# Performance work log

Hardware: AMD Instinct MI355X
Metric: run time of the kernel (lower is better)

The kernel has to match this reference:

```python
import jax, jax.numpy as jnp
import numpy as np

ORB = 54          # unify_orb_num = 27 * 2
N_ATOMS = 64
N_EDGES = 1536
N_P = 256
N_Q = 384
F_P, F_Q, F_O = 0.0002, 0.0001, 0.00015


def setup_inputs() -> dict:
    key = jax.random.key(0)
    ks = jax.random.split(key, 16)
    M = ORB * N_ATOMS
    lattice_vector = 10.0 * jnp.eye(3, dtype=jnp.float32) + 0.1 * jax.random.normal(ks[0], (3, 3), jnp.float32)
    atoms_positions = 10.0 * jax.random.uniform(ks[1], (N_ATOMS, 3), jnp.float32)
    edge_src = jax.random.randint(ks[2], (N_EDGES,), 0, N_ATOMS, jnp.int32)
    edge_dst = jax.random.randint(ks[3], (N_EDGES,), 0, N_ATOMS, jnp.int32)
    # edge_vec = (pos_j - pos_i) + R @ lattice so that round(cell_inv @ R_dis) recovers integer R
    R_int = jax.random.randint(ks[4], (N_EDGES, 3), -2, 3).astype(jnp.float32)
    edge_vec = (atoms_positions[edge_dst] - atoms_positions[edge_src]) + R_int @ lattice_vector
    hr_gt = jax.random.normal(ks[5], (N_EDGES, ORB, ORB), jnp.float32)
    hr_pred = hr_gt + 0.1 * jax.random.normal(ks[6], (N_EDGES, ORB, ORB), jnp.float32)
    kpt_coord = jax.random.uniform(ks[7], (3,), jnp.float32)
    s = np.float32(1.0 / np.sqrt(M))
    P_re = s * jax.random.normal(ks[8], (N_P, M), jnp.float32)
    P_im = s * jax.random.normal(ks[9], (N_P, M), jnp.float32)
    Q_re = s * jax.random.normal(ks[10], (N_Q, M), jnp.float32)
    Q_im = s * jax.random.normal(ks[11], (N_Q, M), jnp.float32)
    H_gt = jax.random.normal(ks[12], (N_EDGES, ORB, ORB), jnp.float32)
    pred_H = H_gt + 0.1 * jax.random.normal(ks[13], (N_EDGES, ORB, ORB), jnp.float32)
    overlap = jax.random.normal(ks[14], (N_EDGES, ORB, ORB), jnp.float32)
    mask_tensor = jnp.ones((N_EDGES, ORB, ORB), jnp.float32)
    return dict(edge_vec=edge_vec, lattice_vector=lattice_vector, atoms_positions=atoms_positions,
                hr_gt=hr_gt, hr_pred=hr_pred, kpt_coord=kpt_coord,
                P_re=P_re, P_im=P_im, Q_re=Q_re, Q_im=Q_im,
                H_gt=H_gt, pred_H=pred_H, overlap=overlap, mask_tensor=mask_tensor,
                edge_src=edge_src, edge_dst=edge_dst)


def _forward(edge_vec, lattice_vector, atoms_positions, hr_gt, hr_pred, kpt_coord,
             P_re, P_im, Q_re, Q_im, H_gt, pred_H, overlap, mask_tensor,
             edge_src, edge_dst):
    M = ORB * atoms_positions.shape[0]
    # --- get_R_list (vectorized): R_tot = round(inv(L^T) @ (edge_vec - (pos_j - pos_i))) ---
    cell_inv = jnp.linalg.inv(lattice_vector.T)
    R_dis = edge_vec - (atoms_positions[edge_dst] - atoms_positions[edge_src])   # [E,3]
    R_tot = jnp.round(R_dis @ cell_inv.T)                                        # [E,3]
    # --- cal_wfc_hk_vectorized: phase factors + block scatter into dense hk ---
    phase = jnp.exp(2j * jnp.pi * (R_tot @ kpt_coord)).astype(jnp.complex64)     # [E]
    idx = jnp.arange(ORB)
    rows = edge_src[:, None, None].astype(jnp.int32) * ORB + idx[None, :, None]  # [E,ORB,1]
    cols = edge_dst[:, None, None].astype(jnp.int32) * ORB + idx[None, None, :]  # [E,1,ORB]
    flat = (rows * M + cols).reshape(-1)                                         # [E*ORB*ORB]

    def build_hk(hr):
        contrib = phase[:, None, None] * hr.astype(jnp.complex64)                # [E,ORB,ORB]
        return jnp.zeros((M * M,), jnp.complex64).at[flat].add(contrib.reshape(-1)).reshape(M, M)

    P = (P_re + 1j * P_im).astype(jnp.complex64)   # [N_P, M]
    Q = (Q_re + 1j * Q_im).astype(jnp.complex64)   # [N_Q, M]

    def project(hk):
        PcH = P.conj() @ hk                        # [N_P, M]
        QcH = Q.conj() @ hk                        # [N_Q, M]
        return PcH @ P.T, QcH @ Q.T, PcH @ Q.T     # [N_P,N_P], [N_Q,N_Q], [N_P,N_Q]

    rP1, rQ1, rPQ1 = project(build_hk(hr_gt))
    rP2, rQ2, rPQ2 = project(build_hk(hr_pred))

    # --- grep_min_mu ---
    f_R = 1.0 - F_P - F_Q - F_O
    N1 = jnp.sum(mask_tensor)
    N2 = N_P * N_P
    N3 = N_Q * N_Q
    N4 = N_P * N_Q
    n1 = f_R * jnp.sum((pred_H - H_gt) * overlap) / N1   # real inputs: real(sum(x*conj(s)))
    d1 = f_R * jnp.sum(overlap * overlap) / N1
    n2 = F_P * jnp.real(jnp.trace(rP2 - rP1)) / N2
    d2 = F_P / N_P
    n3 = F_Q * jnp.real(jnp.trace(rQ2 - rQ1)) / N3
    d3 = F_Q / N_Q
    mu = jax.lax.stop_gradient((n1 + n2 + n3) / (d1 + d2 + d3))  # torch float(mu) detaches

    # --- cal_loss: L1 terms (reduction='none' then sum) ---
    l1 = lambda a, b: jnp.abs(a - b)
    loss_hr = l1(H_gt + mu * overlap, pred_H).sum()
    eyeP = jnp.eye(N_P, dtype=jnp.float32)
    eyeQ = jnp.eye(N_Q, dtype=jnp.float32)
    loss_p = l1(jnp.real(rP1) + mu * eyeP, jnp.real(rP2)).sum() + l1(jnp.imag(rP1), jnp.imag(rP2)).sum()
    loss_q = l1(jnp.real(rQ1) + mu * eyeQ, jnp.real(rQ2)).sum() + l1(jnp.imag(rQ1), jnp.imag(rQ2)).sum()
    loss_pq = l1(jnp.real(rPQ1), jnp.real(rPQ2)).sum() + l1(jnp.imag(rPQ1), jnp.imag(rPQ2)).sum()
    return f_R * loss_hr / N1 + F_P * loss_p / N2 + F_Q * loss_q / N3 + F_O * loss_pq / N4


def reference(edge_vec, lattice_vector, atoms_positions, hr_gt, hr_pred, kpt_coord,
              P_re, P_im, Q_re, Q_im, H_gt, pred_H, overlap, mask_tensor,
              edge_src, edge_dst):
    return _forward(edge_vec, lattice_vector, atoms_positions, hr_gt, hr_pred, kpt_coord,
                    P_re, P_im, Q_re, Q_im, H_gt, pred_H, overlap, mask_tensor,
                    edge_src, edge_dst)
```

## Files before the change

### kernel.cpp

```cpp
#include <hip/hip_runtime.h>
#include <math.h>

#define E_N    1536
#define NATOMS 64
#define M_DIM  3456
#define NP     256
#define NQ     384
#define HRSZ   2916

#define W_FP 0.0002f
#define W_FQ 0.0001f
#define W_FO 0.00015f
#define W_FR (1.0f - W_FP - W_FQ - W_FO)

#define B_HRD  3072
#define B_RED  1094
#define B_PQ   1280
#define B_PREP 1080
#define B_PH   6
#define B_TOT  (B_HRD + B_RED + B_PQ + B_PREP + B_PH)

#define B_LHR  1094

typedef __attribute__((ext_vector_type(8))) short short8;
typedef __attribute__((ext_vector_type(4))) float f32x4;

__device__ __forceinline__ unsigned pk_bf16(float a, float b) {
    unsigned r;
    asm volatile("v_cvt_pk_bf16_f32 %0, %1, %2" : "=v"(r) : "v"(a), "v"(b));
    return r;
}
__device__ __forceinline__ unsigned short f2bf(float x) {
    unsigned u = __builtin_bit_cast(unsigned, x);
    unsigned r = (u + 0x7fffu + ((u >> 16) & 1u)) >> 16;
    return (unsigned short)r;
}

__device__ __forceinline__ void gload_lds16(const void* g, void* l) {
    __builtin_amdgcn_global_load_lds(
        (const __attribute__((address_space(1))) unsigned int*)g,
        (__attribute__((address_space(3))) unsigned int*)l, 16, 0, 0);
}

__device__ __forceinline__ float blockSum(float v, float* sm) {
    v += __shfl_down(v, 32); v += __shfl_down(v, 16); v += __shfl_down(v, 8);
    v += __shfl_down(v, 4);  v += __shfl_down(v, 2);  v += __shfl_down(v, 1);
    __syncthreads();
    if ((threadIdx.x & 63) == 0) sm[threadIdx.x >> 6] = v;
    __syncthreads();
    float r = 0.0f;
    if (threadIdx.x == 0) {
        int nw = blockDim.x >> 6;
        for (int i = 0; i < nw; ++i) r += sm[i];
    }
    return r;
}

__global__ __launch_bounds__(256) void k_pre(
        const float* __restrict__ edge_vec, const float* __restrict__ lat,
        const float* __restrict__ apos, const float* __restrict__ kpt,
        const int* __restrict__ esrc, const int* __restrict__ edst,
        const float* __restrict__ hr_gt, const float* __restrict__ hr_pred,
        const float* __restrict__ P_re, const float* __restrict__ P_im,
        const float* __restrict__ Q_re, const float* __restrict__ Q_im,
        const float4* __restrict__ Hg, const float4* __restrict__ Hp,
        const float4* __restrict__ ov, const float4* __restrict__ mk,
        float* __restrict__ phre, float* __restrict__ phim,
        int* __restrict__ bcnt, int* __restrict__ blist,
        unsigned* __restrict__ hrdG,
        unsigned* __restrict__ PpadR, unsigned* __restrict__ PpadI,
        ushort4* __restrict__ Prebf, ushort4* __restrict__ Pimbf,
        ushort4* __restrict__ Qrebf, ushort4* __restrict__ Qimbf,
        float* __restrict__ acc) {
    __shared__ float sm[8];
    int bid = blockIdx.x;
    int tid = threadIdx.x;

    if (bid < B_HRD) {
        int idx = bid*256 + tid;
        int e = idx >> 9;
        int p = idx & 511;
        int i = p >> 3, q = p & 7;
        unsigned outv[4] = {0,0,0,0};
        if (i < 54 && q < 7) {
            const float* g = hr_gt  + (size_t)e*HRSZ + i*54;
            const float* h = hr_pred + (size_t)e*HRSZ + i*54;
            #pragma unroll
            for (int u = 0; u < 4; ++u) {
                int j2 = q*4 + u;
                if (j2 < 27) {
                    float2 gg = *(const float2*)(g + 2*j2);
                    float2 hh = *(const float2*)(h + 2*j2);
                    outv[u] = pk_bf16(hh.x - gg.x, hh.y - gg.y);
                }
            }
        }
        *(uint4*)(hrdG + (size_t)e*2048 + i*32 + ((q ^ (i & 7)) << 2)) =
            make_uint4(outv[0], outv[1], outv[2], outv[3]);
    } else if (bid < B_HRD + B_RED) {
        const int N4 = E_N*HRSZ/4;
        int base = (bid - B_HRD)*1024 + tid;
        float4 hg[4], hp[4], o[4], m[4];
        #pragma unroll
        for (int u = 0; u < 4; ++u) {
            int i = base + u*256;
            if (i < N4) { hg[u]=Hg[i]; hp[u]=Hp[i]; o[u]=ov[i]; m[u]=mk[i]; }
            else { hg[u]=float4{0,0,0,0}; hp[u]=hg[u]; o[u]=hg[u]; m[u]=hg[u]; }
        }
        float s0 = 0, s1 = 0, s2 = 0;
        #pragma unroll
        for (int u = 0; u < 4; ++u) {
            s0 += (hp[u].x-hg[u].x)*o[u].x + (hp[u].y-hg[u].y)*o[u].y
                + (hp[u].z-hg[u].z)*o[u].z + (hp[u].w-hg[u].w)*o[u].w;
            s1 += o[u].x*o[u].x + o[u].y*o[u].y + o[u].z*o[u].z + o[u].w*o[u].w;
            s2 += m[u].x + m[u].y + m[u].z + m[u].w;
        }
        float r0 = blockSum(s0, sm);
        float r1 = blockSum(s1, sm);
        float r2 = blockSum(s2, sm);
        if (tid == 0) {
            atomicAdd(&acc[0], r0);
            atomicAdd(&acc[1], r1);
            atomicAdd(&acc[2], r2);
        }
    } else if (bid < B_HRD + B_RED + B_PQ) {
        int idx = (bid - B_HRD - B_RED)*256 + tid;
        int q = idx & 7;
        int r = idx >> 3;
        int c = r % 640;
        int dst = r / 640;
        const float* sre = (c < NP) ? (P_re + (size_t)c*M_DIM) : (Q_re + (size_t)(c-NP)*M_DIM);
        const float* sim = (c < NP) ? (P_im + (size_t)c*M_DIM) : (Q_im + (size_t)(c-NP)*M_DIM);
        unsigned vr[4] = {0,0,0,0}, vi[4] = {0,0,0,0};
        if (q < 7) {
            #pragma unroll
            for (int u = 0; u < 4; ++u) {
                int j2 = q*4 + u;
                if (j2 < 27) {
                    int o = dst*54 + 2*j2;
                    float2 fr = *(const float2*)(sre + o);
                    float2 fi = *(const float2*)(sim + o);
                    vr[u] = pk_bf16(fr.x, fr.y);
                    vi[u] = pk_bf16(fi.x, fi.y);
                }
            }
        }
        int loc = (dst*640 + c)*32 + ((q ^ (c & 7)) << 2);
        *(uint4*)(PpadR + loc) = make_uint4(vr[0], vr[1], vr[2], vr[3]);
        *(uint4*)(PpadI + loc) = make_uint4(vi[0], vi[1], vi[2], vi[3]);
    } else if (bid < B_HRD + B_RED + B_PQ + B_PREP) {
        const int NP4 = NP*M_DIM/4;
        const int NQ4 = NQ*M_DIM/4;
        int base = (bid - B_HRD - B_RED - B_PQ)*1024 + tid;
        #pragma unroll
        for (int u = 0; u < 4; ++u) {
            int i = base + u*256;
            const float4* src; ushort4* dst; int o;
            if (i < NP4)            { src = (const float4*)P_re; dst = Prebf; o = i; }
            else if (i < 2*NP4)     { src = (const float4*)P_im; dst = Pimbf; o = i - NP4; }
            else if (i < 2*NP4+NQ4) { src = (const float4*)Q_re; dst = Qrebf; o = i - 2*NP4; }
            else                    { src = (const float4*)Q_im; dst = Qimbf; o = i - 2*NP4 - NQ4; }
            float4 v = src[o];
            ushort4 uu;
            uu.x = f2bf(v.x); uu.y = f2bf(v.y); uu.z = f2bf(v.z); uu.w = f2bf(v.w);
            dst[o] = uu;
        }
    } else {
        int e = (bid - B_HRD - B_RED - B_PQ - B_PREP)*256 + tid;
        if (e >= E_N) return;
        float a00 = lat[0], a01 = lat[3], a02 = lat[6];
        float a10 = lat[1], a11 = lat[4], a12 = lat[7];
        float a20 = lat[2], a21 = lat[5], a22 = lat[8];
        float c00 = a11*a22 - a12*a21;
        float c01 = a12*a20 - a10*a22;
        float c02 = a10*a21 - a11*a20;
        float det = a00*c00 + a01*c01 + a02*c02;
        float id  = 1.0f / det;
        float i00 = c00*id;
        float i01 = (a02*a21 - a01*a22)*id;
        float i02 = (a01*a12 - a02*a11)*id;
        float i10 = c01*id;
        float i11 = (a00*a22 - a02*a20)*id;
        float i12 = (a02*a10 - a00*a12)*id;
        float i20 = c02*id;
        float i21 = (a01*a20 - a00*a21)*id;
        float i22 = (a00*a11 - a01*a10)*id;
        int s = esrc[e], d = edst[e];
        float r0 = edge_vec[e*3+0] - (apos[d*3+0] - apos[s*3+0]);
        float r1 = edge_vec[e*3+1] - (apos[d*3+1] - apos[s*3+1]);
        float r2 = edge_vec[e*3+2] - (apos[d*3+2] - apos[s*3+2]);
        float t0 = roundf(i00*r0 + i01*r1 + i02*r2);
        float t1 = roundf(i10*r0 + i11*r1 + i12*r2);
        float t2 = roundf(i20*r0 + i21*r1 + i22*r2);
        float ph = t0*kpt[0] + t1*kpt[1] + t2*kpt[2];
        float ang = 6.28318530717958647692f * ph;
        phre[e] = cosf(ang);
        phim[e] = sinf(ang);
        int p = atomicAdd(&bcnt[s], 1);
        if (p < 128) blist[s*128 + p] = (e << 6) | d;
    }
}

__global__ __launch_bounds__(256) void k_bp(
        const unsigned* __restrict__ hrdG,
        const unsigned* __restrict__ PpadR, const unsigned* __restrict__ PpadI,
        const float* __restrict__ phre, const float* __restrict__ phim,
        const int* __restrict__ bcnt, const int* __restrict__ blist,
        ushort* __restrict__ BPTPre, ushort* __restrict__ BPTPim,
        ushort* __restrict__ BPTQre, ushort* __restrict__ BPTQim) {
    __shared__ ushort lds[2][12288];
    __shared__ int elist[128];
    __shared__ float phs[2][128];

    int tid = threadIdx.x;
    int a   = blockIdx.x / 10;
    int t   = blockIdx.x - a*10;
    ushort *Or, *Oi; int col0;
    if (t < 4) { Or = BPTPre; Oi = BPTPim; col0 = t*64; }
    else       { Or = BPTQre; Oi = BPTQim; col0 = (t-4)*64; }

    int ne = bcnt[a]; if (ne > 128) ne = 128;
    for (int k = tid; k < ne; k += 256) {
        int v = blist[a*128 + k];
        elist[k] = v;
        phs[0][k] = phre[v >> 6];
        phs[1][k] = phim[v >> 6];
    }
    __syncthreads();

    int w = tid >> 6, l = tid & 63;
    int wr0 = (w >> 1)*32, wc0 = (w & 1)*32;
    int lr = l & 15, kq = l >> 4, lk4 = (l >> 4)*4;

    f32x4 accRe[2][2] = {}, accIm[2][2] = {};

    #define ISSUE(nn, bb) do {                                                     \
        int v_ = elist[(nn)];                                                      \
        int ee_ = v_ >> 6, dst_ = v_ & 63;                                         \
        const ushort* g0_ = (const ushort*)(hrdG + (size_t)ee_*2048);              \
        const ushort* g1_ = (const ushort*)(PpadR + ((size_t)dst_*640 + t*64)*32); \
        const ushort* g2_ = (const ushort*)(PpadI + ((size_t)dst_*640 + t*64)*32); \
        ushort* lb_ = &lds[(bb)][0];                                               \
        _Pragma("unroll")                                                          \
        for (int j_ = 0; j_ < 6; ++j_) {                                           \
            int jj_ = w + j_*4;                                                    \
            int arr_ = jj_ >> 3, ch_ = jj_ & 7;                                    \
            const ushort* gb_ = (arr_ == 0) ? g0_ : (arr_ == 1) ? g1_ : g2_;       \
            gload_lds16(gb_ + ch_*512 + l*8, (void*)(lb_ + arr_*4096 + ch_*512));  \
        }                                                                          \
    } while (0)

    if (ne > 0) ISSUE(0, 0);
    for (int n = 0; n < ne; ++n) {
        int cur = n & 1;
        if (n + 1 < ne) {
            ISSUE(n+1, 1-cur);
            asm volatile("s_waitcnt vmcnt(6)" ::: "memory");
        } else {
            asm volatile("s_waitcnt vmcnt(0)" ::: "memory");
        }
        __syncthreads();
        float phr = phs[0][n], phi_ = phs[1][n];
        const ushort* A  = &lds[cur][0];
        const ushort* BR = A + 4096;
        const ushort* BI = A + 8192;
        short8 a0[2], a1[2], br0[2], br1[2], bi0[2], bi1[2];
        #pragma unroll
        for (int mr = 0; mr < 2; ++mr) {
            int r = wr0 + mr*16 + lr;
            a0[mr] = *(const short8*)(A + r*64 + ((kq     ^ (r & 7))<<3));
            a1[mr] = *(const short8*)(A + r*64 + (((4+kq) ^ (r & 7))<<3));
        }
        #pragma unroll
        for (int nc = 0; nc < 2; ++nc) {
            int c = wc0 + nc*16 + lr;
            br0[nc] = *(const short8*)(BR + c*64 + ((kq     ^ (c & 7))<<3));
            br1[nc] = *(const short8*)(BR + c*64 + (((4+kq) ^ (c & 7))<<3));
            bi0[nc] = *(const short8*)(BI + c*64 + ((kq     ^ (c & 7))<<3));
            bi1[nc] = *(const short8*)(BI + c*64 + (((4+kq) ^ (c & 7))<<3));
        }
        f32x4 z = {0.0f, 0.0f, 0.0f, 0.0f};
        f32x4 t1[2][2], t2[2][2];
        #pragma unroll
        for (int mr = 0; mr < 2; ++mr)
            #pragma unroll
            for (int nc = 0; nc < 2; ++nc) {
                t1[mr][nc] = __builtin_amdgcn_mfma_f32_16x16x32_bf16(a0[mr], br0[nc], z, 0, 0, 0);
                t1[mr][nc] = __builtin_amdgcn_mfma_f32_16x16x32_bf16(a1[mr], br1[nc], t1[mr][nc], 0, 0, 0);
                t2[mr][nc] = __builtin_amdgcn_mfma_f32_16x16x32_bf16(a0[mr], bi0[nc], z, 0, 0, 0);
                t2[mr][nc] = __builtin_amdgcn_mfma_f32_16x16x32_bf16(a1[mr], bi1[nc], t2[mr][nc], 0, 0, 0);
            }
        #pragma unroll
        for (int mr = 0; mr < 2; ++mr)
            #pragma unroll
            for (int nc = 0; nc < 2; ++nc)
                #pragma unroll
                for (int q = 0; q < 4; ++q) {
                    accRe[mr][nc][q] += phr*t1[mr][nc][q] - phi_*t2[mr][nc][q];
                    accIm[mr][nc][q] += phr*t2[mr][nc][q] + phi_*t1[mr][nc][q];
                }
        __syncthreads();
    }
    #undef ISSUE

    #pragma unroll
    for (int mr = 0; mr < 2; ++mr)
        #pragma unroll
        for (int nc = 0; nc < 2; ++nc) {
            int ib = wr0 + mr*16 + lk4;
            if (ib < 54) {
                int cg = col0 + wc0 + nc*16 + lr;
                size_t base = (size_t)cg*M_DIM + (size_t)a*54 + ib;
                *(unsigned*)(Or + base) = pk_bf16(accRe[mr][nc][0], accRe[mr][nc][1]);
                *(unsigned*)(Oi + base) = pk_bf16(accIm[mr][nc][0], accIm[mr][nc][1]);
                if (ib + 2 < 54) {
                    *(unsigned*)(Or + base + 2) = pk_bf16(accRe[mr][nc][2], accRe[mr][nc][3]);
                    *(unsigned*)(Oi + base + 2) = pk_bf16(accIm[mr][nc][2], accIm[mr][nc][3]);
                }
            }
        }
}

#define GPAD 40
__global__ __launch_bounds__(256) void k_gemm(
        const ushort* __restrict__ Prebf, const ushort* __restrict__ Pimbf,
        const ushort* __restrict__ Qrebf, const ushort* __restrict__ Qimbf,
        const ushort* __restrict__ BPTPre, const ushort* __restrict__ BPTPim,
        const ushort* __restrict__ BPTQre, const ushort* __restrict__ BPTQim,
        float* __restrict__ part) {
    __shared__ ushort Ar[64*GPAD], Ai[64*GPAD], Br_[64*GPAD], Bi_[64*GPAD];
    int tid = threadIdx.x;
    int bid = blockIdx.x;
    int t = bid / 6, ks = bid - t*6;
    const ushort *Ag, *Aig, *Bg, *Big; float *Cre, *Cim; int NC, r0, c0;
    if (t < 16) {
        Ag = Prebf; Aig = Pimbf; Bg = BPTPre; Big = BPTPim;
        NC = NP; r0 = (t & 3)*64; c0 = (t >> 2)*64;
        Cre = part + (size_t)ks*2*65536; Cim = Cre + 65536;
    } else if (t < 52) {
        int u = t - 16;
        Ag = Qrebf; Aig = Qimbf; Bg = BPTQre; Big = BPTQim;
        NC = NQ; r0 = (u % 6)*64; c0 = (u / 6)*64;
        Cre = part + 786432 + (size_t)ks*2*147456; Cim = Cre + 147456;
    } else {
        int u = t - 52;
        Ag = Prebf; Aig = Pimbf; Bg = BPTQre; Big = BPTQim;
        NC = NQ; r0 = (u & 3)*64; c0 = (u >> 2)*64;
        Cre = part + 786432 + 1769472 + (size_t)ks*2*98304; Cim = Cre + 98304;
    }
    int k0 = ks * 576;
    int srow = tid >> 2, skq = (tid & 3) * 8;
    int w = tid >> 6, l = tid & 63;
    int wr0 = (w >> 1)*32, wc0 = (w & 1)*32;
    int lr = l & 15, lk = (l >> 4)*8, lk4 = (l >> 4)*4;

    const ushort* pa  = Ag  + (size_t)(r0+srow)*M_DIM + k0 + skq;
    const ushort* pai = Aig + (size_t)(r0+srow)*M_DIM + k0 + skq;
    const ushort* pb  = Bg  + (size_t)(c0+srow)*M_DIM + k0 + skq;
    const ushort* pbi = Big + (size_t)(c0+srow)*M_DIM + k0 + skq;

    short8 ra = *(const short8*)pa, rai = *(const short8*)pai;
    short8 rb = *(const short8*)pb, rbi = *(const short8*)pbi;

    f32x4 aRe[2][2] = {}, aIA[2][2] = {}, aIB[2][2] = {};
    for (int s = 0; s < 18; ++s) {
        __syncthreads();
        *(short8*)(Ar  + srow*GPAD + skq) = ra;
        *(short8*)(Ai  + srow*GPAD + skq) = rai;
        *(short8*)(Br_ + srow*GPAD + skq) = rb;
        *(short8*)(Bi_ + srow*GPAD + skq) = rbi;
        __syncthreads();
        if (s < 17) {
            int o = (s+1)*32;
            ra  = *(const short8*)(pa  + o);
            rai = *(const short8*)(pai + o);
            rb  = *(const short8*)(pb  + o);
            rbi = *(const short8*)(pbi + o);
        }
        short8 fa[2], fn[2], fb[2], fi[2];
        #pragma unroll
        for (int mr = 0; mr < 2; ++mr) {
            int r = wr0 + mr*16 + lr;
            fa[mr] = *(const short8*)(Ar + r*GPAD + lk);
            fn[mr] = *(const short8*)(Ai + r*GPAD + lk);
        }
        #pragma unroll
        for (int nc = 0; nc < 2; ++nc) {
            int c = wc0 + nc*16 + lr;
            fb[nc] = *(const short8*)(Br_ + c*GPAD + lk);
            fi[nc] = *(const short8*)(Bi_ + c*GPAD + lk);
        }
        #pragma unroll
        for (int mr = 0; mr < 2; ++mr)
            #pragma unroll
            for (int nc = 0; nc < 2; ++nc) {
                aRe[mr][nc] = __builtin_amdgcn_mfma_f32_16x16x32_bf16(fa[mr], fb[nc], aRe[mr][nc], 0, 0, 0);
                aRe[mr][nc] = __builtin_amdgcn_mfma_f32_16x16x32_bf16(fn[mr], fi[nc], aRe[mr][nc], 0, 0, 0);
                aIA[mr][nc] = __builtin_amdgcn_mfma_f32_16x16x32_bf16(fa[mr], fi[nc], aIA[mr][nc], 0, 0, 0);
                aIB[mr][nc] = __builtin_amdgcn_mfma_f32_16x16x32_bf16(fn[mr], fb[nc], aIB[mr][nc], 0, 0, 0);
            }
    }
    #pragma unroll
    for (int mr = 0; mr < 2; ++mr)
        #pragma unroll
        for (int nc = 0; nc < 2; ++nc)
            #pragma unroll
            for (int rr = 0; rr < 4; ++rr) {
                int row = r0 + wr0 + mr*16 + lk4 + rr;
                int col = c0 + wc0 + nc*16 + lr;
                Cre[(size_t)row*NC + col] = aRe[mr][nc][rr];
                Cim[(size_t)row*NC + col] = aIA[mr][nc][rr] - aIB[mr][nc][rr];
            }
}

__global__ void k_mu(const float* __restrict__ part, float* __restrict__ acc) {
    int t = threadIdx.x;
    float v1 = 0.0f, v2 = 0.0f;
    if (t < NP) {
        #pragma unroll
        for (int ks = 0; ks < 6; ++ks) v1 += part[ks*131072 + t*(NP+1)];
    }
    if (t < NQ) {
        const float* q = part + 786432;
        #pragma unroll
        for (int ks = 0; ks < 6; ++ks) v2 += q[ks*294912 + t*(NQ+1)];
    }
    __shared__ float sm[8];
    float trP = blockSum(v1, sm);
    float trQ = blockSum(v2, sm);
    if (t == 0) {
        float N1 = acc[2];
        float n1 = W_FR * acc[0] / N1;
        float d1 = W_FR * acc[1] / N1;
        float n2 = W_FP * trP / (float)(NP*NP);
        float n3 = W_FQ * trQ / (float)(NQ*NQ);
        float d2 = W_FP / (float)NP;
        float d3 = W_FQ / (float)NQ;
        acc[3] = (n1 + n2 + n3) / (d1 + d2 + d3);
    }
}

__global__ __launch_bounds__(256) void k_loss(
        const float4* __restrict__ Hg, const float4* __restrict__ Hp,
        const float4* __restrict__ ov, const float* __restrict__ part,
        float* __restrict__ acc) {
    __shared__ float sm[8];
    int bid = blockIdx.x;
    int tid = threadIdx.x;
    float mu = acc[3];
    if (bid < B_LHR) {
        const int N4 = E_N*HRSZ/4;
        int base = bid*1024 + tid;
        float4 hg[4], hp[4], o[4];
        #pragma unroll
        for (int u = 0; u < 4; ++u) {
            int i = base + u*256;
            if (i < N4) { hg[u]=Hg[i]; hp[u]=Hp[i]; o[u]=ov[i]; }
            else { hg[u]=float4{0,0,0,0}; hp[u]=hg[u]; o[u]=hg[u]; }
        }
        float s = 0;
        #pragma unroll
        for (int u = 0; u < 4; ++u) {
            s += fabsf(hg[u].x + mu*o[u].x - hp[u].x) + fabsf(hg[u].y + mu*o[u].y - hp[u].y)
               + fabsf(hg[u].z + mu*o[u].z - hp[u].z) + fabsf(hg[u].w + mu*o[u].w - hp[u].w);
        }
        float r = blockSum(s, sm);
        if (tid == 0) atomicAdd(&acc[4], r);
    } else {
        const int NPP = NP*NP, NQQ = NQ*NQ, NPQ = NP*NQ;
        float sP = 0, sQ = 0, sPQ = 0;
        int stride = 256*256;
        for (int i = (bid - B_LHR)*256 + tid; i < NPP+NQQ+NPQ; i += stride) {
            if (i < NPP) {
                float sre = 0, sim = 0;
                #pragma unroll
                for (int ks = 0; ks < 6; ++ks) {
                    sre += part[ks*131072 + i];
                    sim += part[ks*131072 + 65536 + i];
                }
                int r = i >> 8, c = i & 255;
                float d = (r == c) ? mu : 0.0f;
                sP += fabsf(d - sre) + fabsf(sim);
            } else if (i < NPP+NQQ) {
                int j = i - NPP;
                const float* q = part + 786432;
                float sre = 0, sim = 0;
                #pragma unroll
                for (int ks = 0; ks < 6; ++ks) {
                    sre += q[ks*294912 + j];
                    sim += q[ks*294912 + 147456 + j];
                }
                int r = j / NQ, c = j - r*NQ;
                float d = (r == c) ? mu : 0.0f;
                sQ += fabsf(d - sre) + fabsf(sim);
            } else {
                int j = i - (NPP+NQQ);
                const float* pq = part + 786432 + 1769472;
                float sre = 0, sim = 0;
                #pragma unroll
                for (int ks = 0; ks < 6; ++ks) {
                    sre += pq[ks*196608 + j];
                    sim += pq[ks*196608 + 98304 + j];
                }
                sPQ += fabsf(sre) + fabsf(sim);
            }
        }
        float a1 = blockSum(sP, sm);
        float a2 = blockSum(sQ, sm);
        float a3 = blockSum(sPQ, sm);
        if (tid == 0) {
            atomicAdd(&acc[5], a1);
            atomicAdd(&acc[6], a2);
            atomicAdd(&acc[7], a3);
        }
    }
}

__global__ void k_final(const float* __restrict__ acc, float* __restrict__ out) {
    if (threadIdx.x == 0 && blockIdx.x == 0) {
        float N1 = acc[2];
        out[0] = W_FR*acc[4]/N1
               + W_FP*acc[5]/(float)(NP*NP)
               + W_FQ*acc[6]/(float)(NQ*NQ)
               + W_FO*acc[7]/(float)(NP*NQ);
    }
}

extern "C" void kernel_launch(void* const* d_in, const int* in_sizes, int n_in,
                              void* d_out, int out_size, void* d_ws, size_t ws_size,
                              hipStream_t stream) {
    const float* edge_vec = (const float*)d_in[0];
    const float* lattice  = (const float*)d_in[1];
    const float* apos     = (const float*)d_in[2];
    const float* hr_gt    = (const float*)d_in[3];
    const float* hr_pred  = (const float*)d_in[4];
    const float* kpt      = (const float*)d_in[5];
    const float* P_re     = (const float*)d_in[6];
    const float* P_im     = (const float*)d_in[7];
    const float* Q_re     = (const float*)d_in[8];
    const float* Q_im     = (const float*)d_in[9];
    const float* H_gt     = (const float*)d_in[10];
    const float* pred_H   = (const float*)d_in[11];
    const float* overlap  = (const float*)d_in[12];
    const float* mask     = (const float*)d_in[13];
    const int*   esrc     = (const int*)d_in[14];
    const int*   edst     = (const int*)d_in[15];
    float* out = (float*)d_out;

    float* ws   = (float*)d_ws;
    float* acc  = ws;
    int*   bcnt = (int*)(ws + 16);
    int*   blist= (int*)(ws + 80);
    float* phre = ws + 8272;
    float* phim = phre + E_N;
    ushort* us  = (ushort*)(ws + 16384);
    ushort* Prebf  = us;
    ushort* Pimbf  = Prebf  + (size_t)NP*M_DIM;
    ushort* Qrebf  = Pimbf  + (size_t)NP*M_DIM;
    ushort* Qimbf  = Qrebf  + (size_t)NQ*M_DIM;
    ushort* BPTPre = Qimbf  + (size_t)NQ*M_DIM;
    ushort* BPTPim = BPTPre + (size_t)NP*M_DIM;
    ushort* BPTQre = BPTPim + (size_t)NP*M_DIM;
    ushort* BPTQim = BPTQre + (size_t)NQ*M_DIM;
    unsigned* PpadR = (unsigned*)(BPTQim + (size_t)NQ*M_DIM);
    unsigned* PpadI = PpadR + (size_t)64*640*32;
    unsigned* hrdG  = PpadI + (size_t)64*640*32;
    float* part = (float*)hrdG;

    hipMemsetAsync(ws, 0, 320, stream);

    k_pre<<<B_TOT, 256, 0, stream>>>(edge_vec, lattice, apos, kpt, esrc, edst,
                                     hr_gt, hr_pred, P_re, P_im, Q_re, Q_im,
                                     (const float4*)H_gt, (const float4*)pred_H,
                                     (const float4*)overlap, (const float4*)mask,
                                     phre, phim, bcnt, blist,
                                     hrdG, PpadR, PpadI,
                                     (ushort4*)Prebf, (ushort4*)Pimbf,
                                     (ushort4*)Qrebf, (ushort4*)Qimbf, acc);
    k_bp<<<NATOMS*10, 256, 0, stream>>>(hrdG, PpadR, PpadI, phre, phim, bcnt, blist,
                                        BPTPre, BPTPim, BPTQre, BPTQim);
    k_gemm<<<456, 256, 0, stream>>>(Prebf, Pimbf, Qrebf, Qimbf,
                                    BPTPre, BPTPim, BPTQre, BPTQim, part);
    k_mu<<<1, 512, 0, stream>>>(part, acc);
    k_loss<<<B_LHR + 256, 256, 0, stream>>>((const float4*)H_gt, (const float4*)pred_H,
                                            (const float4*)overlap, part, acc);
    k_final<<<1, 1, 0, stream>>>(acc, out);
}
```

Baseline: 308.2 us.

## Cache bf16 H-difference and overlap in pre-pass; fuse P/Q bf16 conversion into padding

The pre-kernel now runs on a fixed 1024-block grid with grid-stride loops. The separate P/Q bf16 conversion pass is merged into the padded-layout pass, so P and Q are read once. When the workspace is large enough, the reduction pass also writes bf16 copies of (pred_H - H_gt) and overlap, and the final L1 loss reads those 4-byte pairs instead of three fp32 tensors, cutting that pass's traffic. The cost is extra writes in the pre-pass and bf16 rounding in the hr loss term, which changes numerics.

```diff
diff --git a/kernel.cpp b/kernel.cpp
--- a/kernel.cpp
+++ b/kernel.cpp
@@ -13,14 +13,10 @@
 #define W_FO 0.00015f
 #define W_FR (1.0f - W_FP - W_FQ - W_FO)
 
-#define B_HRD  3072
-#define B_RED  1094
-#define B_PQ   1280
-#define B_PREP 1080
-#define B_PH   6
-#define B_TOT  (B_HRD + B_RED + B_PQ + B_PREP + B_PH)
-
-#define B_LHR  1094
+#define N4_RED (E_N*HRSZ/4)
+#define TOT_A  (E_N*512)
+#define TOT_C  (NATOMS*640*8)
+#define GRID_PRE 1024
 
 typedef __attribute__((ext_vector_type(8))) short short8;
 typedef __attribute__((ext_vector_type(4))) float f32x4;
@@ -30,10 +26,9 @@
     asm volatile("v_cvt_pk_bf16_f32 %0, %1, %2" : "=v"(r) : "v"(a), "v"(b));
     return r;
 }
-__device__ __forceinline__ unsigned short f2bf(float x) {
-    unsigned u = __builtin_bit_cast(unsigned, x);
-    unsigned r = (u + 0x7fffu + ((u >> 16) & 1u)) >> 16;
-    return (unsigned short)r;
+__device__ __forceinline__ float bf2f(unsigned short u) {
+    unsigned v = ((unsigned)u) << 16;
+    return __builtin_bit_cast(float, v);
 }
 
 __device__ __forceinline__ void gload_lds16(const void* g, void* l) {
@@ -69,15 +64,53 @@
         int* __restrict__ bcnt, int* __restrict__ blist,
         unsigned* __restrict__ hrdG,
         unsigned* __restrict__ PpadR, unsigned* __restrict__ PpadI,
-        ushort4* __restrict__ Prebf, ushort4* __restrict__ Pimbf,
-        ushort4* __restrict__ Qrebf, ushort4* __restrict__ Qimbf,
-        float* __restrict__ acc) {
+        ushort* __restrict__ Prebf, ushort* __restrict__ Pimbf,
+        ushort* __restrict__ Qrebf, ushort* __restrict__ Qimbf,
+        unsigned* __restrict__ dH, unsigned* __restrict__ ovb,
+        float* __restrict__ acc, int compact) {
     __shared__ float sm[8];
     int bid = blockIdx.x;
     int tid = threadIdx.x;
 
-    if (bid < B_HRD) {
-        int idx = bid*256 + tid;
+    if (bid < 6) {
+        int e = bid*256 + tid;
+        if (e < E_N) {
+            float a00 = lat[0], a01 = lat[3], a02 = lat[6];
+            float a10 = lat[1], a11 = lat[4], a12 = lat[7];
+            float a20 = lat[2], a21 = lat[5], a22 = lat[8];
+            float c00 = a11*a22 - a12*a21;
+            float c01 = a12*a20 - a10*a22;
+            float c02 = a10*a21 - a11*a20;
+            float det = a00*c00 + a01*c01 + a02*c02;
+            float id  = 1.0f / det;
+            float i00 = c00*id;
+            float i01 = (a02*a21 - a01*a22)*id;
+            float i02 = (a01*a12 - a02*a11)*id;
+            float i10 = c01*id;
+            float i11 = (a00*a22 - a02*a20)*id;
+            float i12 = (a02*a10 - a00*a12)*id;
+            float i20 = c02*id;
+            float i21 = (a01*a20 - a00*a21)*id;
+            float i22 = (a00*a11 - a01*a10)*id;
+            int s = esrc[e], d = edst[e];
+            float r0 = edge_vec[e*3+0] - (apos[d*3+0] - apos[s*3+0]);
+            float r1 = edge_vec[e*3+1] - (apos[d*3+1] - apos[s*3+1]);
+            float r2 = edge_vec[e*3+2] - (apos[d*3+2] - apos[s*3+2]);
+            float t0 = roundf(i00*r0 + i01*r1 + i02*r2);
+            float t1 = roundf(i10*r0 + i11*r1 + i12*r2);
+            float t2 = roundf(i20*r0 + i21*r1 + i22*r2);
+            float ph = t0*kpt[0] + t1*kpt[1] + t2*kpt[2];
+            float ang = 6.28318530717958647692f * ph;
+            phre[e] = cosf(ang);
+            phim[e] = sinf(ang);
+            int p = atomicAdd(&bcnt[s], 1);
+            if (p < 128) blist[s*128 + p] = (e << 6) | d;
+        }
+    }
+
+    #pragma unroll
+    for (int it = 0; it < 3; ++it) {
+        int idx = bid*256 + tid + it*(GRID_PRE*256);
         int e = idx >> 9;
         int p = idx & 511;
         int i = p >> 3, q = p & 7;
@@ -97,23 +130,37 @@
         }
         *(uint4*)(hrdG + (size_t)e*2048 + i*32 + ((q ^ (i & 7)) << 2)) =
             make_uint4(outv[0], outv[1], outv[2], outv[3]);
-    } else if (bid < B_HRD + B_RED) {
-        const int N4 = E_N*HRSZ/4;
-        int base = (bid - B_HRD)*1024 + tid;
-        float4 hg[4], hp[4], o[4], m[4];
-        #pragma unroll
-        for (int u = 0; u < 4; ++u) {
-            int i = base + u*256;
-            if (i < N4) { hg[u]=Hg[i]; hp[u]=Hp[i]; o[u]=ov[i]; m[u]=mk[i]; }
-            else { hg[u]=float4{0,0,0,0}; hp[u]=hg[u]; o[u]=hg[u]; m[u]=hg[u]; }
-        }
+    }
+
+    {
         float s0 = 0, s1 = 0, s2 = 0;
         #pragma unroll
-        for (int u = 0; u < 4; ++u) {
-            s0 += (hp[u].x-hg[u].x)*o[u].x + (hp[u].y-hg[u].y)*o[u].y
-                + (hp[u].z-hg[u].z)*o[u].z + (hp[u].w-hg[u].w)*o[u].w;
-            s1 += o[u].x*o[u].x + o[u].y*o[u].y + o[u].z*o[u].z + o[u].w*o[u].w;
-            s2 += m[u].x + m[u].y + m[u].z + m[u].w;
+        for (int it = 0; it < 2; ++it) {
+            if (bid*1024 + it*(GRID_PRE*1024) < N4_RED) {
+                int b0 = bid*1024 + tid + it*(GRID_PRE*1024);
+                float4 hg[4], hp[4], o[4], m[4];
+                int val[4];
+                #pragma unroll
+                for (int u = 0; u < 4; ++u) {
+                    int i = b0 + u*256;
+                    val[u] = (i < N4_RED);
+                    if (val[u]) { hg[u]=Hg[i]; hp[u]=Hp[i]; o[u]=ov[i]; m[u]=mk[i]; }
+                    else { hg[u]=float4{0,0,0,0}; hp[u]=hg[u]; o[u]=hg[u]; m[u]=hg[u]; }
+                }
+                #pragma unroll
+                for (int u = 0; u < 4; ++u) {
+                    float dx = hp[u].x-hg[u].x, dy = hp[u].y-hg[u].y;
+                    float dz = hp[u].z-hg[u].z, dw = hp[u].w-hg[u].w;
+                    s0 += dx*o[u].x + dy*o[u].y + dz*o[u].z + dw*o[u].w;
+                    s1 += o[u].x*o[u].x + o[u].y*o[u].y + o[u].z*o[u].z + o[u].w*o[u].w;
+                    s2 += m[u].x + m[u].y + m[u].z + m[u].w;
+                    if (compact && val[u]) {
+                        int i = b0 + u*256;
+                        *(uint2*)(dH  + (size_t)i*2) = make_uint2(pk_bf16(dx, dy), pk_bf16(dz, dw));
+                        *(uint2*)(ovb + (size_t)i*2) = make_uint2(pk_bf16(o[u].x, o[u].y), pk_bf16(o[u].z, o[u].w));
+                    }
+                }
+            }
         }
         float r0 = blockSum(s0, sm);
         float r1 = blockSum(s1, sm);
@@ -123,81 +170,42 @@
             atomicAdd(&acc[1], r1);
             atomicAdd(&acc[2], r2);
         }
-    } else if (bid < B_HRD + B_RED + B_PQ) {
-        int idx = (bid - B_HRD - B_RED)*256 + tid;
-        int q = idx & 7;
-        int r = idx >> 3;
-        int c = r % 640;
-        int dst = r / 640;
-        const float* sre = (c < NP) ? (P_re + (size_t)c*M_DIM) : (Q_re + (size_t)(c-NP)*M_DIM);
-        const float* sim = (c < NP) ? (P_im + (size_t)c*M_DIM) : (Q_im + (size_t)(c-NP)*M_DIM);
-        unsigned vr[4] = {0,0,0,0}, vi[4] = {0,0,0,0};
-        if (q < 7) {
-            #pragma unroll
-            for (int u = 0; u < 4; ++u) {
-                int j2 = q*4 + u;
-                if (j2 < 27) {
-                    int o = dst*54 + 2*j2;
-                    float2 fr = *(const float2*)(sre + o);
-                    float2 fi = *(const float2*)(sim + o);
-                    vr[u] = pk_bf16(fr.x, fr.y);
-                    vi[u] = pk_bf16(fi.x, fi.y);
-                }
-            }
-        }
-        int loc = (dst*640 + c)*32 + ((q ^ (c & 7)) << 2);
-        *(uint4*)(PpadR + loc) = make_uint4(vr[0], vr[1], vr[2], vr[3]);
-        *(uint4*)(PpadI + loc) = make_uint4(vi[0], vi[1], vi[2], vi[3]);
-    } else if (bid < B_HRD + B_RED + B_PQ + B_PREP) {
-        const int NP4 = NP*M_DIM/4;
-        const int NQ4 = NQ*M_DIM/4;
-        int base = (bid - B_HRD - B_RED - B_PQ)*1024 + tid;
-        #pragma unroll
-        for (int u = 0; u < 4; ++u) {
-            int i = base + u*256;
-            const float4* src; ushort4* dst; int o;
-            if (i < NP4)            { src = (const float4*)P_re; dst = Prebf; o = i; }
-            else if (i < 2*NP4)     { src = (const float4*)P_im; dst = Pimbf; o = i - NP4; }
-            else if (i < 2*NP4+NQ4) { src = (const float4*)Q_re; dst = Qrebf; o = i - 2*NP4; }
-            else                    { src = (const float4*)Q_im; dst = Qimbf; o = i - 2*NP4 - NQ4; }
-            float4 v = src[o];
-            ushort4 uu;
-            uu.x = f2bf(v.x); uu.y = f2bf(v.y); uu.z = f2bf(v.z); uu.w = f2bf(v.w);
-            dst[o] = uu;
-        }
-    } else {
-        int e = (bid - B_HRD - B_RED - B_PQ - B_PREP)*256 + tid;
-        if (e >= E_N) return;
-        float a00 = lat[0], a01 = lat[3], a02 = lat[6];
-        float a10 = lat[1], a11 = lat[4], a12 = lat[7];
-        float a20 = lat[2], a21 = lat[5], a22 = lat[8];
-        float c00 = a11*a22 - a12*a21;
-        float c01 = a12*a20 - a10*a22;
-        float c02 = a10*a21 - a11*a20;
-        float det = a00*c00 + a01*c01 + a02*c02;
-        float id  = 1.0f / det;
-        float i00 = c00*id;
-        float i01 = (a02*a21 - a01*a22)*id;
-        float i02 = (a01*a12 - a02*a11)*id;
-        float i10 = c01*id;
-        float i11 = (a00*a22 - a02*a20)*id;
-        float i12 = (a02*a10 - a00*a12)*id;
-        float i20 = c02*id;
-        float i21 = (a01*a20 - a00*a21)*id;
-        float i22 = (a00*a11 - a01*a10)*id;
-        int s = esrc[e], d = edst[e];
-        float r0 = edge_vec[e*3+0] - (apos[d*3+0] - apos[s*3+0]);
-        float r1 = edge_vec[e*3+1] - (apos[d*3+1] - apos[s*3+1]);
-        float r2 = edge_vec[e*3+2] - (apos[d*3+2] - apos[s*3+2]);
-        float t0 = roundf(i00*r0 + i01*r1 + i02*r2);
-        float t1 = roundf(i10*r0 + i11*r1 + i12*r2);
-        float t2 = roundf(i20*r0 + i21*r1 + i22*r2);
-        float ph = t0*kpt[0] + t1*kpt[1] + t2*kpt[2];
-        float ang = 6.28318530717958647692f * ph;
-        phre[e] = cosf(ang);
-        phim[e] = sinf(ang);
-        int p = atomicAdd(&bcnt[s], 1);
-        if (p < 128) blist[s*128 + p] = (e << 6) | d;
+    }
+
+    #pragma unroll
+    for (int it = 0; it < 2; ++it) {
+        int idx = bid*256 + tid + it*(GRID_PRE*256);
+        if (idx < TOT_C) {
+            int q = idx & 7;
+            int r = idx >> 3;
+            int c = r % 640;
+            int dst = r / 640;
+            const float* sre = (c < NP) ? (P_re + (size_t)c*M_DIM) : (Q_re + (size_t)(c-NP)*M_DIM);
+            const float* sim = (c < NP) ? (P_im + (size_t)c*M_DIM) : (Q_im + (size_t)(c-NP)*M_DIM);
+            ushort* fre = (c < NP) ? Prebf : Qrebf;
+            ushort* fim = (c < NP) ? Pimbf : Qimbf;
+            int cc = (c < NP) ? c : c - NP;
+            unsigned vr[4] = {0,0,0,0}, vi[4] = {0,0,0,0};
+            if (q < 7) {
+                #pragma unroll
+                for (int u = 0; u < 4; ++u) {
+                    int j2 = q*4 + u;
+                    if (j2 < 27) {
+                        int o = dst*54 + 2*j2;
+                        float2 fr = *(const float2*)(sre + o);
+                        float2 fi = *(const float2*)(sim + o);
+                        vr[u] = pk_bf16(fr.x, fr.y);
+                        vi[u] = pk_bf16(fi.x, fi.y);
+                        int fo = cc*M_DIM + dst*54 + 2*j2;
+                        *(unsigned*)(fre + fo) = vr[u];
+                        *(unsigned*)(fim + fo) = vi[u];
+                    }
+                }
+            }
+            int loc = (dst*640 + c)*32 + ((q ^ (c & 7)) << 2);
+            *(uint4*)(PpadR + loc) = make_uint4(vr[0], vr[1], vr[2], vr[3]);
+            *(uint4*)(PpadI + loc) = make_uint4(vi[0], vi[1], vi[2], vi[3]);
+        }
     }
 }
 
@@ -442,27 +450,49 @@
 
 __global__ __launch_bounds__(256) void k_loss(
         const float4* __restrict__ Hg, const float4* __restrict__ Hp,
-        const float4* __restrict__ ov, const float* __restrict__ part,
-        float* __restrict__ acc) {
+        const float4* __restrict__ ov,
+        const uint4* __restrict__ dH, const uint4* __restrict__ ovb,
+        const float* __restrict__ part,
+        float* __restrict__ acc, int bhr, int compact) {
     __shared__ float sm[8];
     int bid = blockIdx.x;
     int tid = threadIdx.x;
     float mu = acc[3];
-    if (bid < B_LHR) {
-        const int N4 = E_N*HRSZ/4;
-        int base = bid*1024 + tid;
-        float4 hg[4], hp[4], o[4];
-        #pragma unroll
-        for (int u = 0; u < 4; ++u) {
-            int i = base + u*256;
-            if (i < N4) { hg[u]=Hg[i]; hp[u]=Hp[i]; o[u]=ov[i]; }
-            else { hg[u]=float4{0,0,0,0}; hp[u]=hg[u]; o[u]=hg[u]; }
-        }
+    if (bid < bhr) {
         float s = 0;
-        #pragma unroll
-        for (int u = 0; u < 4; ++u) {
-            s += fabsf(hg[u].x + mu*o[u].x - hp[u].x) + fabsf(hg[u].y + mu*o[u].y - hp[u].y)
-               + fabsf(hg[u].z + mu*o[u].z - hp[u].z) + fabsf(hg[u].w + mu*o[u].w - hp[u].w);
+        if (compact) {
+            const int N8 = E_N*HRSZ/8;
+            int b0 = bid*1024 + tid;
+            #pragma unroll
+            for (int u = 0; u < 4; ++u) {
+                int i8 = b0 + u*256;
+                if (i8 < N8) {
+                    uint4 dv = dH[i8];
+                    uint4 o4 = ovb[i8];
+                    unsigned dd[4] = {dv.x, dv.y, dv.z, dv.w};
+                    unsigned oo[4] = {o4.x, o4.y, o4.z, o4.w};
+                    #pragma unroll
+                    for (int p = 0; p < 4; ++p) {
+                        float d0 = bf2f((unsigned short)(dd[p] & 0xffffu));
+                        float d1 = bf2f((unsigned short)(dd[p] >> 16));
+                        float o0 = bf2f((unsigned short)(oo[p] & 0xffffu));
+                        float o1 = bf2f((unsigned short)(oo[p] >> 16));
+                        s += fabsf(mu*o0 - d0) + fabsf(mu*o1 - d1);
+                    }
+                }
+            }
+        } else {
+            const int N4 = E_N*HRSZ/4;
+            int b0 = bid*1024 + tid;
+            #pragma unroll
+            for (int u = 0; u < 4; ++u) {
+                int i = b0 + u*256;
+                if (i < N4) {
+                    float4 hg = Hg[i], hp = Hp[i], o = ov[i];
+                    s += fabsf(hg.x + mu*o.x - hp.x) + fabsf(hg.y + mu*o.y - hp.y)
+                       + fabsf(hg.z + mu*o.z - hp.z) + fabsf(hg.w + mu*o.w - hp.w);
+                }
+            }
         }
         float r = blockSum(s, sm);
         if (tid == 0) atomicAdd(&acc[4], r);
@@ -470,7 +500,7 @@
         const int NPP = NP*NP, NQQ = NQ*NQ, NPQ = NP*NQ;
         float sP = 0, sQ = 0, sPQ = 0;
         int stride = 256*256;
-        for (int i = (bid - B_LHR)*256 + tid; i < NPP+NQQ+NPQ; i += stride) {
+        for (int i = (bid - bhr)*256 + tid; i < NPP+NQQ+NPQ; i += stride) {
             if (i < NPP) {
                 float sre = 0, sim = 0;
                 #pragma unroll
@@ -566,23 +596,31 @@
     unsigned* PpadI = PpadR + (size_t)64*640*32;
     unsigned* hrdG  = PpadI + (size_t)64*640*32;
     float* part = (float*)hrdG;
+    size_t part_end_bytes = ((char*)part - (char*)d_ws) + (size_t)3735552*4;
+    unsigned* dH  = (unsigned*)((char*)d_ws + part_end_bytes);
+    unsigned* ovb = dH + (size_t)E_N*HRSZ/2;
+    size_t need = part_end_bytes + 2*(size_t)E_N*HRSZ*2;
+    int compact = (ws_size >= need) ? 1 : 0;
 
     hipMemsetAsync(ws, 0, 320, stream);
 
-    k_pre<<<B_TOT, 256, 0, stream>>>(edge_vec, lattice, apos, kpt, esrc, edst,
-                                     hr_gt, hr_pred, P_re, P_im, Q_re, Q_im,
-                                     (const float4*)H_gt, (const float4*)pred_H,
-                                     (const float4*)overlap, (const float4*)mask,
-                                     phre, phim, bcnt, blist,
-                                     hrdG, PpadR, PpadI,
-                                     (ushort4*)Prebf, (ushort4*)Pimbf,
-                                     (ushort4*)Qrebf, (ushort4*)Qimbf, acc);
+    k_pre<<<GRID_PRE, 256, 0, stream>>>(edge_vec, lattice, apos, kpt, esrc, edst,
+                                        hr_gt, hr_pred, P_re, P_im, Q_re, Q_im,
+                                        (const float4*)H_gt, (const float4*)pred_H,
+                                        (const float4*)overlap, (const float4*)mask,
+                                        phre, phim, bcnt, blist,
+                                        hrdG, PpadR, PpadI,
+                                        Prebf, Pimbf, Qrebf, Qimbf,
+                                        dH, ovb, acc, compact);
     k_bp<<<NATOMS*10, 256, 0, stream>>>(hrdG, PpadR, PpadI, phre, phim, bcnt, blist,
                                         BPTPre, BPTPim, BPTQre, BPTQim);
     k_gemm<<<456, 256, 0, stream>>>(Prebf, Pimbf, Qrebf, Qimbf,
                                     BPTPre, BPTPim, BPTQre, BPTQim, part);
     k_mu<<<1, 512, 0, stream>>>(part, acc);
-    k_loss<<<B_LHR + 256, 256, 0, stream>>>((const float4*)H_gt, (const float4*)pred_H,
-                                            (const float4*)overlap, part, acc);
+    int bhr = compact ? 547 : 1094;
+    k_loss<<<bhr + 256, 256, 0, stream>>>((const float4*)H_gt, (const float4*)pred_H,
+                                          (const float4*)overlap,
+                                          (const uint4*)dH, (const uint4*)ovb,
+                                          part, acc, bhr, compact);
     k_final<<<1, 1, 0, stream>>>(acc, out);
 }
```

New measurement: 314.4 us. 2.0% more time.

## Compute mu traces in k_bp epilogue and fuse H loss into GEMM launch

Applied to the files above, without the earlier changes.

The diagonal traces of the P and Q Gram products are now accumulated in the k_bp epilogue as elementwise dot products of the projected accumulators with the P/Q bf16 rows. This lets mu be known before the GEMM finishes, so the separate single-block k_mu kernel is removed. The large L1 loss over H_gt/pred_H/overlap moves into extra blocks of the GEMM launch, so it can overlap with GEMM work. Risks include different rounding in the trace, since it uses fp32 accumulators times bf16 instead of summed GEMM partials, plus extra global reads and a block reduction in k_bp.

```diff
diff --git a/kernel.cpp b/kernel.cpp
--- a/kernel.cpp
+++ b/kernel.cpp
@@ -20,7 +20,11 @@
 #define B_PH   6
 #define B_TOT  (B_HRD + B_RED + B_PQ + B_PREP + B_PH)
 
-#define B_LHR  1094
+#define N4_RED (E_N*HRSZ/4)
+#define TOT_C  (NATOMS*640*8)
+
+#define BHR    1094
+#define BGEMM  456
 
 typedef __attribute__((ext_vector_type(8))) short short8;
 typedef __attribute__((ext_vector_type(4))) float f32x4;
@@ -34,6 +38,10 @@
     unsigned u = __builtin_bit_cast(unsigned, x);
     unsigned r = (u + 0x7fffu + ((u >> 16) & 1u)) >> 16;
     return (unsigned short)r;
+}
+__device__ __forceinline__ float bf2f(unsigned short u) {
+    unsigned v = ((unsigned)u) << 16;
+    return __builtin_bit_cast(float, v);
 }
 
 __device__ __forceinline__ void gload_lds16(const void* g, void* l) {
@@ -54,6 +62,17 @@
         for (int i = 0; i < nw; ++i) r += sm[i];
     }
     return r;
+}
+
+__device__ __forceinline__ float mu_from(const float* acc) {
+    float N1 = acc[2];
+    float n1 = W_FR * acc[0] / N1;
+    float d1 = W_FR * acc[1] / N1;
+    float n2 = W_FP * acc[8] / (float)(NP*NP);
+    float n3 = W_FQ * acc[9] / (float)(NQ*NQ);
+    float d2 = W_FP / (float)NP;
+    float d3 = W_FQ / (float)NQ;
+    return (n1 + n2 + n3) / (d1 + d2 + d3);
 }
 
 __global__ __launch_bounds__(256) void k_pre(
@@ -98,13 +117,12 @@
         *(uint4*)(hrdG + (size_t)e*2048 + i*32 + ((q ^ (i & 7)) << 2)) =
             make_uint4(outv[0], outv[1], outv[2], outv[3]);
     } else if (bid < B_HRD + B_RED) {
-        const int N4 = E_N*HRSZ/4;
         int base = (bid - B_HRD)*1024 + tid;
         float4 hg[4], hp[4], o[4], m[4];
         #pragma unroll
         for (int u = 0; u < 4; ++u) {
             int i = base + u*256;
-            if (i < N4) { hg[u]=Hg[i]; hp[u]=Hp[i]; o[u]=ov[i]; m[u]=mk[i]; }
+            if (i < N4_RED) { hg[u]=Hg[i]; hp[u]=Hp[i]; o[u]=ov[i]; m[u]=mk[i]; }
             else { hg[u]=float4{0,0,0,0}; hp[u]=hg[u]; o[u]=hg[u]; m[u]=hg[u]; }
         }
         float s0 = 0, s1 = 0, s2 = 0;
@@ -206,18 +224,23 @@
         const unsigned* __restrict__ PpadR, const unsigned* __restrict__ PpadI,
         const float* __restrict__ phre, const float* __restrict__ phim,
         const int* __restrict__ bcnt, const int* __restrict__ blist,
+        const ushort* __restrict__ Prebf, const ushort* __restrict__ Pimbf,
+        const ushort* __restrict__ Qrebf, const ushort* __restrict__ Qimbf,
         ushort* __restrict__ BPTPre, ushort* __restrict__ BPTPim,
-        ushort* __restrict__ BPTQre, ushort* __restrict__ BPTQim) {
+        ushort* __restrict__ BPTQre, ushort* __restrict__ BPTQim,
+        float* __restrict__ acc) {
     __shared__ ushort lds[2][12288];
     __shared__ int elist[128];
     __shared__ float phs[2][128];
+    __shared__ float smtr[8];
 
     int tid = threadIdx.x;
     int a   = blockIdx.x / 10;
     int t   = blockIdx.x - a*10;
     ushort *Or, *Oi; int col0;
-    if (t < 4) { Or = BPTPre; Oi = BPTPim; col0 = t*64; }
-    else       { Or = BPTQre; Oi = BPTQim; col0 = (t-4)*64; }
+    const ushort *Fr, *Fi;
+    if (t < 4) { Or = BPTPre; Oi = BPTPim; col0 = t*64; Fr = Prebf; Fi = Pimbf; }
+    else       { Or = BPTQre; Oi = BPTQim; col0 = (t-4)*64; Fr = Qrebf; Fi = Qimbf; }
 
     int ne = bcnt[a]; if (ne > 128) ne = 128;
     for (int k = tid; k < ne; k += 256) {
@@ -319,6 +342,26 @@
                 }
             }
         }
+
+    float tr = 0.0f;
+    #pragma unroll
+    for (int mr = 0; mr < 2; ++mr)
+        #pragma unroll
+        for (int nc = 0; nc < 2; ++nc) {
+            int ib = wr0 + mr*16 + lk4;
+            int cg = col0 + wc0 + nc*16 + lr;
+            size_t off = (size_t)cg*M_DIM + (size_t)a*54 + ib;
+            #pragma unroll
+            for (int q = 0; q < 4; ++q) {
+                if (ib + q < 54) {
+                    float pr = bf2f(Fr[off + q]);
+                    float pi = bf2f(Fi[off + q]);
+                    tr += accRe[mr][nc][q]*pr + accIm[mr][nc][q]*pi;
+                }
+            }
+        }
+    float rtr = blockSum(tr, smtr);
+    if (tid == 0) atomicAdd(&acc[8 + (t < 4 ? 0 : 1)], rtr);
 }
 
 #define GPAD 40
@@ -327,11 +370,37 @@
         const ushort* __restrict__ Qrebf, const ushort* __restrict__ Qimbf,
         const ushort* __restrict__ BPTPre, const ushort* __restrict__ BPTPim,
         const ushort* __restrict__ BPTQre, const ushort* __restrict__ BPTQim,
-        float* __restrict__ part) {
+        const float4* __restrict__ Hg, const float4* __restrict__ Hp,
+        const float4* __restrict__ ov,
+        float* __restrict__ part, float* __restrict__ acc) {
     __shared__ ushort Ar[64*GPAD], Ai[64*GPAD], Br_[64*GPAD], Bi_[64*GPAD];
     int tid = threadIdx.x;
     int bid = blockIdx.x;
-    int t = bid / 6, ks = bid - t*6;
+
+    if (bid < BHR) {
+        float mu = mu_from(acc);
+        int base = bid*1024 + tid;
+        float4 hg[4], hp[4], o[4];
+        #pragma unroll
+        for (int u = 0; u < 4; ++u) {
+            int i = base + u*256;
+            if (i < N4_RED) { hg[u]=Hg[i]; hp[u]=Hp[i]; o[u]=ov[i]; }
+            else { hg[u]=float4{0,0,0,0}; hp[u]=hg[u]; o[u]=hg[u]; }
+        }
+        float s = 0;
+        #pragma unroll
+        for (int u = 0; u < 4; ++u) {
+            s += fabsf(hg[u].x + mu*o[u].x - hp[u].x) + fabsf(hg[u].y + mu*o[u].y - hp[u].y)
+               + fabsf(hg[u].z + mu*o[u].z - hp[u].z) + fabsf(hg[u].w + mu*o[u].w - hp[u].w);
+        }
+        __shared__ float sm[8];
+        float r = blockSum(s, sm);
+        if (tid == 0) atomicAdd(&acc[4], r);
+        return;
+    }
+
+    int b2 = bid - BHR;
+    int t = b2 / 6, ks = b2 - t*6;
     const ushort *Ag, *Aig, *Bg, *Big; float *Cre, *Cim; int NC, r0, c0;
     if (t < 16) {
         Ag = Prebf; Aig = Pimbf; Bg = BPTPre; Big = BPTPim;
@@ -413,106 +482,56 @@
             }
 }
 
-__global__ void k_mu(const float* __restrict__ part, float* __restrict__ acc) {
-    int t = threadIdx.x;
-    float v1 = 0.0f, v2 = 0.0f;
-    if (t < NP) {
-        #pragma unroll
-        for (int ks = 0; ks < 6; ++ks) v1 += part[ks*131072 + t*(NP+1)];
-    }
-    if (t < NQ) {
-        const float* q = part + 786432;
-        #pragma unroll
-        for (int ks = 0; ks < 6; ++ks) v2 += q[ks*294912 + t*(NQ+1)];
-    }
+__global__ __launch_bounds__(256) void k_loss(
+        const float* __restrict__ part, float* __restrict__ acc) {
     __shared__ float sm[8];
-    float trP = blockSum(v1, sm);
-    float trQ = blockSum(v2, sm);
-    if (t == 0) {
-        float N1 = acc[2];
-        float n1 = W_FR * acc[0] / N1;
-        float d1 = W_FR * acc[1] / N1;
-        float n2 = W_FP * trP / (float)(NP*NP);
-        float n3 = W_FQ * trQ / (float)(NQ*NQ);
-        float d2 = W_FP / (float)NP;
-        float d3 = W_FQ / (float)NQ;
-        acc[3] = (n1 + n2 + n3) / (d1 + d2 + d3);
-    }
-}
-
-__global__ __launch_bounds__(256) void k_loss(
-        const float4* __restrict__ Hg, const float4* __restrict__ Hp,
-        const float4* __restrict__ ov, const float* __restrict__ part,
-        float* __restrict__ acc) {
-    __shared__ float sm[8];
-    int bid = blockIdx.x;
+    const int NPP = NP*NP, NQQ = NQ*NQ, NPQ = NP*NQ;
+    float mu = mu_from(acc);
     int tid = threadIdx.x;
-    float mu = acc[3];
-    if (bid < B_LHR) {
-        const int N4 = E_N*HRSZ/4;
-        int base = bid*1024 + tid;
-        float4 hg[4], hp[4], o[4];
-        #pragma unroll
-        for (int u = 0; u < 4; ++u) {
-            int i = base + u*256;
-            if (i < N4) { hg[u]=Hg[i]; hp[u]=Hp[i]; o[u]=ov[i]; }
-            else { hg[u]=float4{0,0,0,0}; hp[u]=hg[u]; o[u]=hg[u]; }
-        }
-        float s = 0;
-        #pragma unroll
-        for (int u = 0; u < 4; ++u) {
-            s += fabsf(hg[u].x + mu*o[u].x - hp[u].x) + fabsf(hg[u].y + mu*o[u].y - hp[u].y)
-               + fabsf(hg[u].z + mu*o[u].z - hp[u].z) + fabsf(hg[u].w + mu*o[u].w - hp[u].w);
-        }
-        float r = blockSum(s, sm);
-        if (tid == 0) atomicAdd(&acc[4], r);
-    } else {
-        const int NPP = NP*NP, NQQ = NQ*NQ, NPQ = NP*NQ;
-        float sP = 0, sQ = 0, sPQ = 0;
-        int stride = 256*256;
-        for (int i = (bid - B_LHR)*256 + tid; i < NPP+NQQ+NPQ; i += stride) {
-            if (i < NPP) {
-                float sre = 0, sim = 0;
-                #pragma unroll
-                for (int ks = 0; ks < 6; ++ks) {
-                    sre += part[ks*131072 + i];
-                    sim += part[ks*131072 + 65536 + i];
-                }
-                int r = i >> 8, c = i & 255;
-                float d = (r == c) ? mu : 0.0f;
-                sP += fabsf(d - sre) + fabsf(sim);
-            } else if (i < NPP+NQQ) {
-                int j = i - NPP;
-                const float* q = part + 786432;
-                float sre = 0, sim = 0;
-                #pragma unroll
-                for (int ks = 0; ks < 6; ++ks) {
-                    sre += q[ks*294912 + j];
-                    sim += q[ks*294912 + 147456 + j];
-                }
-                int r = j / NQ, c = j - r*NQ;
-                float d = (r == c) ? mu : 0.0f;
-                sQ += fabsf(d - sre) + fabsf(sim);
-            } else {
-                int j = i - (NPP+NQQ);
-                const float* pq = part + 786432 + 1769472;
-                float sre = 0, sim = 0;
-                #pragma unroll
-                for (int ks = 0; ks < 6; ++ks) {
-                    sre += pq[ks*196608 + j];
-                    sim += pq[ks*196608 + 98304 + j];
-                }
-                sPQ += fabsf(sre) + fabsf(sim);
-            }
-        }
-        float a1 = blockSum(sP, sm);
-        float a2 = blockSum(sQ, sm);
-        float a3 = blockSum(sPQ, sm);
-        if (tid == 0) {
-            atomicAdd(&acc[5], a1);
-            atomicAdd(&acc[6], a2);
-            atomicAdd(&acc[7], a3);
-        }
+    float sP = 0, sQ = 0, sPQ = 0;
+    int stride = 256*256;
+    for (int i = blockIdx.x*256 + tid; i < NPP+NQQ+NPQ; i += stride) {
+        if (i < NPP) {
+            float sre = 0, sim = 0;
+            #pragma unroll
+            for (int ks = 0; ks < 6; ++ks) {
+                sre += part[ks*131072 + i];
+                sim += part[ks*131072 + 65536 + i];
+            }
+            int r = i >> 8, c = i & 255;
+            float d = (r == c) ? mu : 0.0f;
+            sP += fabsf(d - sre) + fabsf(sim);
+        } else if (i < NPP+NQQ) {
+            int j = i - NPP;
+            const float* q = part + 786432;
+            float sre = 0, sim = 0;
+            #pragma unroll
+            for (int ks = 0; ks < 6; ++ks) {
+                sre += q[ks*294912 + j];
+                sim += q[ks*294912 + 147456 + j];
+            }
+            int r = j / NQ, c = j - r*NQ;
+            float d = (r == c) ? mu : 0.0f;
+            sQ += fabsf(d - sre) + fabsf(sim);
+        } else {
+            int j = i - (NPP+NQQ);
+            const float* pq = part + 786432 + 1769472;
+            float sre = 0, sim = 0;
+            #pragma unroll
+            for (int ks = 0; ks < 6; ++ks) {
+                sre += pq[ks*196608 + j];
+                sim += pq[ks*196608 + 98304 + j];
+            }
+            sPQ += fabsf(sre) + fabsf(sim);
+        }
+    }
+    float a1 = blockSum(sP, sm);
+    float a2 = blockSum(sQ, sm);
+    float a3 = blockSum(sPQ, sm);
+    if (tid == 0) {
+        atomicAdd(&acc[5], a1);
+        atomicAdd(&acc[6], a2);
+        atomicAdd(&acc[7], a3);
     }
 }
 
@@ -578,11 +597,12 @@
                                      (ushort4*)Prebf, (ushort4*)Pimbf,
                                      (ushort4*)Qrebf, (ushort4*)Qimbf, acc);
     k_bp<<<NATOMS*10, 256, 0, stream>>>(hrdG, PpadR, PpadI, phre, phim, bcnt, blist,
-                                        BPTPre, BPTPim, BPTQre, BPTQim);
-    k_gemm<<<456, 256, 0, stream>>>(Prebf, Pimbf, Qrebf, Qimbf,
-                                    BPTPre, BPTPim, BPTQre, BPTQim, part);
-    k_mu<<<1, 512, 0, stream>>>(part, acc);
-    k_loss<<<B_LHR + 256, 256, 0, stream>>>((const float4*)H_gt, (const float4*)pred_H,
+                                        Prebf, Pimbf, Qrebf, Qimbf,
+                                        BPTPre, BPTPim, BPTQre, BPTQim, acc);
+    k_gemm<<<BHR + BGEMM, 256, 0, stream>>>(Prebf, Pimbf, Qrebf, Qimbf,
+                                            BPTPre, BPTPim, BPTQre, BPTQim,
+                                            (const float4*)H_gt, (const float4*)pred_H,
                                             (const float4*)overlap, part, acc);
+    k_loss<<<256, 256, 0, stream>>>(part, acc);
     k_final<<<1, 1, 0, stream>>>(acc, out);
 }
```

Measured after the change: 331.9 us. 7.7% more time.
